# Kernel tuning notes

Hardware: AMD Instinct MI355X
Metric: run time of the kernel (lower is better)

Reference implementation:

```python
import jax, jax.numpy as jnp
import numpy as np

B, LQ, LK, DQ, DKEY, DV = 8, 2048, 2048, 1024, 1024, 1024
MASK_NEG = -1e6  # d2l masked_softmax fill value


def setup_inputs() -> dict:
    key = jax.random.key(0)
    kq, kk, kv, kl, kw = jax.random.split(key, 5)
    queries = jax.random.normal(kq, (B, LQ, DQ), dtype=jnp.float32)
    keys = jax.random.normal(kk, (B, LK, DKEY), dtype=jnp.float32)
    values = jax.random.normal(kv, (B, LK, DV), dtype=jnp.float32)
    valid_lens = jax.random.randint(kl, (B,), 1, LK + 1)
    W_q = jax.random.normal(kw, (DQ, DKEY), dtype=jnp.float32) / np.sqrt(DQ)
    return {"queries": queries, "keys": keys, "values": values,
            "valid_lens": valid_lens, "W_q": W_q}


def reference(queries, keys, values, valid_lens, W_q):
    # Q projection: LazyLinear(key_dim, bias=False)
    q = jnp.einsum("bqd,dk->bqk", queries, W_q)          # [B, LQ, DKEY]
    d = q.shape[-1]
    scores = jnp.einsum("bqk,bsk->bqs", q, keys) / jnp.sqrt(jnp.asarray(d, q.dtype))
    # masked_softmax: positions >= valid_len set to -1e6 before softmax
    mask = jnp.arange(scores.shape[-1])[None, None, :] < valid_lens[:, None, None]
    scores = jnp.where(mask, scores, MASK_NEG)
    attn = jax.nn.softmax(scores, axis=-1)               # [B, LQ, LK]
    # dropout p=0.0 (eval) -> identity
    return jnp.einsum("bqs,bsv->bqv", attn, values)      # [B, LQ, DV]
```

## Files before the change

kernel.cpp:

```cpp
#include <hip/hip_runtime.h>
#include <cstdint>
#include <cstddef>

#define B_   8
#define LQ_  2048
#define LK_  2048

typedef __attribute__((ext_vector_type(8))) __bf16 bf16x8;
typedef __attribute__((ext_vector_type(4))) float f32x4;
typedef __attribute__((ext_vector_type(8))) unsigned short ushortx8;

__device__ __forceinline__ unsigned short f2bf(float f) {
  unsigned u = __builtin_bit_cast(unsigned, f);
  u = u + 0x7fffu + ((u >> 16) & 1u);
  return (unsigned short)(u >> 16);
}
__device__ __forceinline__ float bf2f(unsigned short h) {
  unsigned u = ((unsigned)h) << 16;
  return __builtin_bit_cast(float, u);
}

__device__ __forceinline__ void gld_lds16(const void* g, void* l) {
  __builtin_amdgcn_global_load_lds((__attribute__((address_space(1))) void*)(void*)g,
                                   (__attribute__((address_space(3))) void*)l, 16, 0, 0);
}

__global__ __launch_bounds__(256) void cast_kw_kernel(
    const float* __restrict__ k, unsigned short* __restrict__ ko,
    const float* __restrict__ w, unsigned short* __restrict__ wo,
    const int* __restrict__ vlp) {
  int bb = (int)blockIdx.x;
  const float* in;
  unsigned short* out;
  if (bb < 8192) {
    in = k; out = ko;
    int batch = bb >> 10;
    int row = (bb & 1023) * 2;
    int vl = vlp[batch];
    if (row >= ((vl + 255) & ~255)) return;
  } else {
    bb -= 8192;
    in = w; out = wo;
  }
  size_t i = ((size_t)bb * 256 + threadIdx.x) * 8;
  float4 a = *(const float4*)(in + i);
  float4 b = *(const float4*)(in + i + 4);
  ushortx8 o;
  o[0] = f2bf(a.x); o[1] = f2bf(a.y); o[2] = f2bf(a.z); o[3] = f2bf(a.w);
  o[4] = f2bf(b.x); o[5] = f2bf(b.y); o[6] = f2bf(b.z); o[7] = f2bf(b.w);
  *(ushortx8*)(out + i) = o;
}

template <int OUTM, int SKIPN, int SKIPM, int CLAMPK, int QCAST>
__global__ __launch_bounds__(256, 2) void gemm256x128_kernel(
    const unsigned short* __restrict__ A, const unsigned short* __restrict__ B,
    void* __restrict__ Cp, int M, int N, int K,
    long a_bstride, long b_bstride, long c_bstride, float scale,
    const int* __restrict__ vlp, int lognx,
    const float* __restrict__ qf, unsigned short* __restrict__ qbf, int ngemm) {
  __shared__ unsigned short lds[2][128 * 64 + 64 * 64];

  const int tid = threadIdx.x;

  if constexpr (QCAST) {
    if ((int)blockIdx.x >= ngemm) {
      size_t i = ((size_t)((int)blockIdx.x - ngemm) * 256 + tid) * 8;
      float4 a = *(const float4*)(qf + i);
      float4 b = *(const float4*)(qf + i + 4);
      ushortx8 o;
      o[0] = f2bf(a.x); o[1] = f2bf(a.y); o[2] = f2bf(a.z); o[3] = f2bf(a.w);
      o[4] = f2bf(b.x); o[5] = f2bf(b.y); o[6] = f2bf(b.z); o[7] = f2bf(b.w);
      *(ushortx8*)(qbf + i) = o;
      return;
    }
  }

  const int wid = tid >> 6;
  const int lane = tid & 63;
  const int lane15 = lane & 15;
  const int lhalf = lane >> 4;

  const int idx = (int)blockIdx.x;
  const int z = idx & 7;
  const int rest = idx >> 3;
  const int nxm = (1 << lognx) - 1;
  const int xt = rest & nxm;
  const int yt = rest >> lognx;
  const int nt = (xt + 2 * z) & nxm;
  const int m0 = yt * 256;
  const int n0 = nt * 128;

  int vl = K;
  if constexpr (SKIPN || SKIPM || CLAMPK) vl = vlp[z];
  if constexpr (SKIPN) {
    if (n0 >= vl) return;
  }
  if constexpr (SKIPM) {
    if (m0 >= vl) return;
  }
  int kEnd = K;
  if constexpr (CLAMPK) {
    int ke = (vl + 63) & ~63;
    kEnd = ke < K ? ke : K;
  }
  const int nKt = kEnd >> 5;

  const unsigned short* Ab = A + (size_t)z * a_bstride;
  const unsigned short* Bb = B + (size_t)z * b_bstride;

  int srA[4], scA[4], sdA[4];
#pragma unroll
  for (int j = 0; j < 4; ++j) {
    int blk = (wid * 4 + j) * 64 + lane;
    int p = blk >> 3;
    int c = (blk & 7) ^ (p & 7);
    srA[j] = m0 + 2 * p + (c >> 2);
    scA[j] = (c & 3) * 8;
    sdA[j] = blk * 8;
  }
  int srB[2], scB[2], sdB[2];
#pragma unroll
  for (int j = 0; j < 2; ++j) {
    int blk = (wid * 2 + j) * 64 + lane;
    int p = blk >> 3;
    int c = (blk & 7) ^ (p & 7);
    srB[j] = n0 + 2 * p + (c >> 2);
    scB[j] = (c & 3) * 8;
    sdB[j] = 8192 + blk * 8;
  }

  const int om = (wid & 1) * 128;
  const int on = (wid >> 1) * 64;
  const int swz8 = ((((lane15 & 1) << 2) + lhalf) ^ ((lane15 >> 1) & 7)) << 3;
  const int aBase = ((om >> 1) + (lane15 >> 1)) * 64 + swz8;
  const int bBase = 8192 + ((on >> 1) + (lane15 >> 1)) * 64 + swz8;

  f32x4 acc[8][4];
#pragma unroll
  for (int f = 0; f < 8; ++f)
#pragma unroll
    for (int g = 0; g < 4; ++g) acc[f][g] = (f32x4){0.f, 0.f, 0.f, 0.f};

#define STAGE_TILE(T, S)                                                        \
  {                                                                             \
    const int kc_ = (T) * 32;                                                   \
    _Pragma("unroll")                                                           \
    for (int j = 0; j < 4; ++j)                                                 \
      gld_lds16(Ab + (size_t)srA[j] * K + (kc_ + scA[j]), &lds[S][sdA[j]]);     \
    _Pragma("unroll")                                                           \
    for (int j = 0; j < 2; ++j)                                                 \
      gld_lds16(Bb + (size_t)srB[j] * K + (kc_ + scB[j]), &lds[S][sdB[j]]);     \
  }

  STAGE_TILE(0, 0);
  asm volatile("s_waitcnt vmcnt(0)" ::: "memory");
  __builtin_amdgcn_s_barrier();

  for (int t = 0; t < nKt; ++t) {
    const unsigned short* lcur = &lds[t & 1][0];
    if (t + 1 < nKt) STAGE_TILE(t + 1, (t + 1) & 1);

    bf16x8 a[8], b[4];
#pragma unroll
    for (int f = 0; f < 8; ++f) a[f] = *(const bf16x8*)&lcur[aBase + f * 512];
#pragma unroll
    for (int g = 0; g < 4; ++g) b[g] = *(const bf16x8*)&lcur[bBase + g * 512];
#pragma unroll
    for (int f = 0; f < 8; ++f)
#pragma unroll
      for (int g = 0; g < 4; ++g)
        acc[f][g] = __builtin_amdgcn_mfma_f32_16x16x32_bf16(a[f], b[g], acc[f][g], 0, 0, 0);
    asm volatile("s_waitcnt vmcnt(0)" ::: "memory");
    __builtin_amdgcn_s_barrier();
  }
#undef STAGE_TILE

  const size_t boffC = (size_t)z * c_bstride;
#pragma unroll
  for (int f = 0; f < 8; ++f) {
    int row = m0 + om + f * 16 + lhalf * 4;
#pragma unroll
    for (int g = 0; g < 4; ++g) {
      int col = n0 + on + g * 16 + lane15;
#pragma unroll
      for (int r = 0; r < 4; ++r) {
        float v = acc[f][g][r];
        if constexpr (OUTM == 0) {
          ((unsigned short*)Cp + boffC)[(size_t)(row + r) * N + col] = f2bf(v);
        } else if constexpr (OUTM == 1) {
          ((unsigned short*)Cp + boffC)[(size_t)(row + r) * N + col] = f2bf(v * scale);
        } else {
          ((float*)Cp + boffC)[(size_t)(row + r) * N + col] = v;
        }
      }
    }
  }
}

__global__ __launch_bounds__(256) void vtrans_softmax_kernel(
    const float* __restrict__ vals, unsigned short* __restrict__ valsT,
    unsigned short* __restrict__ scores, const int* __restrict__ valid_lens) {
  __shared__ float smem[32 * 33];
  const int bb = (int)blockIdx.x;
  const int tid = threadIdx.x;

  if (bb < 16384) {
    const int z = bb >> 11;
    const int r0 = ((bb >> 5) & 63) * 32;
    const int kEnd = (valid_lens[z] + 63) & ~63;
    if (r0 >= kEnd) return;
    const int c0 = (bb & 31) * 32;
    const int tx = tid & 31, ty = tid >> 5;
    const float* inb = vals + (size_t)z * 2048 * 1024;
    unsigned short* outb = valsT + (size_t)z * 1024 * 2048;
#pragma unroll
    for (int k = 0; k < 4; ++k) {
      int r = ty + k * 8;
      smem[r * 33 + tx] = inb[(size_t)(r0 + r) * 1024 + c0 + tx];
    }
    __syncthreads();
#pragma unroll
    for (int k = 0; k < 4; ++k) {
      int c = ty + k * 8;
      outb[(size_t)(c0 + c) * 2048 + r0 + tx] = f2bf(smem[tx * 33 + c]);
    }
    return;
  }

  const int row = bb - 16384;
  const int b = row >> 11;
  const int vl = valid_lens[b];
  const int kEnd = (vl + 63) & ~63;
  unsigned short* rp = scores + (size_t)row * LK_;
  const int wid = tid >> 6, lane = tid & 63;
  float* sred = smem;

  const int cb = tid * 8;
  const bool act = cb < kEnd;
  ushortx8 h = {};
  if (act) h = *(const ushortx8*)(rp + cb);
  float x[8];
#pragma unroll
  for (int t = 0; t < 8; ++t) x[t] = bf2f(h[t]);

  float m = -3.4e38f;
#pragma unroll
  for (int t = 0; t < 8; ++t)
    if (cb + t < vl) m = fmaxf(m, x[t]);
#pragma unroll
  for (int off = 32; off >= 1; off >>= 1) m = fmaxf(m, __shfl_xor(m, off));
  if (lane == 0) sred[wid] = m;
  __syncthreads();
  m = fmaxf(fmaxf(sred[0], sred[1]), fmaxf(sred[2], sred[3]));
  __syncthreads();

  float e[8];
  float s = 0.f;
#pragma unroll
  for (int t = 0; t < 8; ++t) {
    e[t] = (cb + t < vl) ? __expf(x[t] - m) : 0.f;
    s += e[t];
  }
#pragma unroll
  for (int off = 32; off >= 1; off >>= 1) s += __shfl_xor(s, off);
  if (lane == 0) sred[wid] = s;
  __syncthreads();
  s = sred[0] + sred[1] + sred[2] + sred[3];
  float inv = 1.f / s;

  if (act) {
    ushortx8 o;
#pragma unroll
    for (int t = 0; t < 8; ++t) o[t] = f2bf(e[t] * inv);
    *(ushortx8*)(rp + cb) = o;
  }
}

extern "C" void kernel_launch(void* const* d_in, const int* in_sizes, int n_in,
                              void* d_out, int out_size, void* d_ws, size_t ws_size,
                              hipStream_t stream) {
  const float* queries = (const float*)d_in[0];
  const float* keys = (const float*)d_in[1];
  const float* values = (const float*)d_in[2];
  const int* valid_lens = (const int*)d_in[3];
  const float* W_q = (const float*)d_in[4];
  float* out = (float*)d_out;

  unsigned short* ws = (unsigned short*)d_ws;
  const size_t M1 = (size_t)1024 * 1024;
  unsigned short* q_bf = ws;
  unsigned short* scores = ws + 16 * M1;
  unsigned short* keysP = ws + 48 * M1;
  unsigned short* valsT = keysP;
  unsigned short* w_bf = ws + 64 * M1;
  unsigned short* keys_bf = ws + 65 * M1;

  cast_kw_kernel<<<dim3(8704), 256, 0, stream>>>(
      keys, keys_bf, W_q, w_bf, valid_lens);
  gemm256x128_kernel<0, 0, 1, 0, 1><<<dim3(512 + 8192), 256, 0, stream>>>(
      keys_bf, w_bf, keysP, 2048, 1024, 1024,
      (long)2048 * 1024, 0, (long)2048 * 1024, 1.f, valid_lens, 3,
      queries, q_bf, 512);
  gemm256x128_kernel<1, 1, 0, 0, 0><<<dim3(8 * 16 * 8), 256, 0, stream>>>(
      q_bf, keysP, scores, 2048, 2048, 1024,
      (long)2048 * 1024, (long)2048 * 1024, (long)2048 * 2048, 0.03125f, valid_lens, 4,
      nullptr, nullptr, 0);
  vtrans_softmax_kernel<<<dim3(32768), 256, 0, stream>>>(
      values, valsT, scores, valid_lens);
  gemm256x128_kernel<2, 0, 0, 1, 0><<<dim3(8 * 8 * 8), 256, 0, stream>>>(
      scores, valsT, out, 2048, 1024, 2048,
      (long)2048 * 2048, (long)1024 * 2048, (long)2048 * 1024, 1.f, valid_lens, 3,
      nullptr, nullptr, 0);
}
```

Baseline: 366.4 us.

## Fuse V transpose-cast into QK^T GEMM launch as auxiliary blocks

Moves the values transpose-and-cast-to-bf16 work out of the softmax kernel and into extra blocks appended to the QK^T score GEMM grid. Each auxiliary block handles eight 32x32 tiles and uses the GEMM's LDS as scratch. The transposed values are written into the keys_bf buffer, which is no longer needed by then, so they no longer alias keysP, which that GEMM is still reading. The aim is to let the bandwidth-bound transpose overlap with the compute-bound GEMM and to leave softmax as a lean kernel. The cost is that the auxiliary blocks compete with GEMM blocks for CU slots, and their fixed block count of 2048 may leave a load-imbalanced tail.

```diff
diff --git a/kernel.cpp b/kernel.cpp
--- a/kernel.cpp
+++ b/kernel.cpp
@@ -51,26 +51,58 @@
   *(ushortx8*)(out + i) = o;
 }
 
-template <int OUTM, int SKIPN, int SKIPM, int CLAMPK, int QCAST>
+template <int OUTM, int SKIPN, int SKIPM, int CLAMPK, int AUX>
 __global__ __launch_bounds__(256, 2) void gemm256x128_kernel(
     const unsigned short* __restrict__ A, const unsigned short* __restrict__ B,
     void* __restrict__ Cp, int M, int N, int K,
     long a_bstride, long b_bstride, long c_bstride, float scale,
     const int* __restrict__ vlp, int lognx,
-    const float* __restrict__ qf, unsigned short* __restrict__ qbf, int ngemm) {
+    const float* __restrict__ auxf, unsigned short* __restrict__ auxo, int ngemm) {
   __shared__ unsigned short lds[2][128 * 64 + 64 * 64];
 
   const int tid = threadIdx.x;
 
-  if constexpr (QCAST) {
+  if constexpr (AUX == 1) {
     if ((int)blockIdx.x >= ngemm) {
       size_t i = ((size_t)((int)blockIdx.x - ngemm) * 256 + tid) * 8;
-      float4 a = *(const float4*)(qf + i);
-      float4 b = *(const float4*)(qf + i + 4);
+      float4 a = *(const float4*)(auxf + i);
+      float4 b = *(const float4*)(auxf + i + 4);
       ushortx8 o;
       o[0] = f2bf(a.x); o[1] = f2bf(a.y); o[2] = f2bf(a.z); o[3] = f2bf(a.w);
       o[4] = f2bf(b.x); o[5] = f2bf(b.y); o[6] = f2bf(b.z); o[7] = f2bf(b.w);
-      *(ushortx8*)(qbf + i) = o;
+      *(ushortx8*)(auxo + i) = o;
+      return;
+    }
+  }
+  if constexpr (AUX == 2) {
+    if ((int)blockIdx.x >= ngemm) {
+      float* smem = (float*)&lds[0][0];
+      const int vb = (int)blockIdx.x - ngemm;
+      const int tx = tid & 31, ty = tid >> 5;
+#pragma unroll 1
+      for (int u = 0; u < 8; ++u) {
+        const int t = vb * 8 + u;
+        const int z = t >> 11;
+        const int r0 = ((t >> 5) & 63) * 32;
+        const int c0 = (t & 31) * 32;
+        const int kEnd = (vlp[z] + 63) & ~63;
+        if (r0 < kEnd) {
+          const float* inb = auxf + (size_t)z * 2048 * 1024;
+          unsigned short* outb = auxo + (size_t)z * 1024 * 2048;
+#pragma unroll
+          for (int k = 0; k < 4; ++k) {
+            int r = ty + k * 8;
+            smem[r * 33 + tx] = inb[(size_t)(r0 + r) * 1024 + c0 + tx];
+          }
+          __syncthreads();
+#pragma unroll
+          for (int k = 0; k < 4; ++k) {
+            int c = ty + k * 8;
+            outb[(size_t)(c0 + c) * 2048 + r0 + tx] = f2bf(smem[tx * 33 + c]);
+          }
+          __syncthreads();
+        }
+      }
       return;
     }
   }
@@ -197,43 +229,16 @@
   }
 }
 
-__global__ __launch_bounds__(256) void vtrans_softmax_kernel(
-    const float* __restrict__ vals, unsigned short* __restrict__ valsT,
-    unsigned short* __restrict__ scores, const int* __restrict__ valid_lens) {
-  __shared__ float smem[32 * 33];
-  const int bb = (int)blockIdx.x;
-  const int tid = threadIdx.x;
-
-  if (bb < 16384) {
-    const int z = bb >> 11;
-    const int r0 = ((bb >> 5) & 63) * 32;
-    const int kEnd = (valid_lens[z] + 63) & ~63;
-    if (r0 >= kEnd) return;
-    const int c0 = (bb & 31) * 32;
-    const int tx = tid & 31, ty = tid >> 5;
-    const float* inb = vals + (size_t)z * 2048 * 1024;
-    unsigned short* outb = valsT + (size_t)z * 1024 * 2048;
-#pragma unroll
-    for (int k = 0; k < 4; ++k) {
-      int r = ty + k * 8;
-      smem[r * 33 + tx] = inb[(size_t)(r0 + r) * 1024 + c0 + tx];
-    }
-    __syncthreads();
-#pragma unroll
-    for (int k = 0; k < 4; ++k) {
-      int c = ty + k * 8;
-      outb[(size_t)(c0 + c) * 2048 + r0 + tx] = f2bf(smem[tx * 33 + c]);
-    }
-    return;
-  }
-
-  const int row = bb - 16384;
+__global__ __launch_bounds__(256) void softmax_kernel(unsigned short* __restrict__ scores,
+                                                      const int* __restrict__ valid_lens) {
+  const int row = blockIdx.x;
   const int b = row >> 11;
   const int vl = valid_lens[b];
   const int kEnd = (vl + 63) & ~63;
   unsigned short* rp = scores + (size_t)row * LK_;
+  const int tid = threadIdx.x;
   const int wid = tid >> 6, lane = tid & 63;
-  float* sred = smem;
+  __shared__ float sred[4];
 
   const int cb = tid * 8;
   const bool act = cb < kEnd;
@@ -291,9 +296,9 @@
   unsigned short* q_bf = ws;
   unsigned short* scores = ws + 16 * M1;
   unsigned short* keysP = ws + 48 * M1;
-  unsigned short* valsT = keysP;
   unsigned short* w_bf = ws + 64 * M1;
   unsigned short* keys_bf = ws + 65 * M1;
+  unsigned short* valsT = keys_bf;
 
   cast_kw_kernel<<<dim3(8704), 256, 0, stream>>>(
       keys, keys_bf, W_q, w_bf, valid_lens);
@@ -301,12 +306,11 @@
       keys_bf, w_bf, keysP, 2048, 1024, 1024,
       (long)2048 * 1024, 0, (long)2048 * 1024, 1.f, valid_lens, 3,
       queries, q_bf, 512);
-  gemm256x128_kernel<1, 1, 0, 0, 0><<<dim3(8 * 16 * 8), 256, 0, stream>>>(
+  gemm256x128_kernel<1, 1, 0, 0, 2><<<dim3(1024 + 2048), 256, 0, stream>>>(
       q_bf, keysP, scores, 2048, 2048, 1024,
       (long)2048 * 1024, (long)2048 * 1024, (long)2048 * 2048, 0.03125f, valid_lens, 4,
-      nullptr, nullptr, 0);
-  vtrans_softmax_kernel<<<dim3(32768), 256, 0, stream>>>(
-      values, valsT, scores, valid_lens);
+      values, valsT, 1024);
+  softmax_kernel<<<dim3(B_ * LQ_), 256, 0, stream>>>(scores, valid_lens);
   gemm256x128_kernel<2, 0, 0, 1, 0><<<dim3(8 * 8 * 8), 256, 0, stream>>>(
       scores, valsT, out, 2048, 1024, 2048,
       (long)2048 * 2048, (long)1024 * 2048, (long)2048 * 1024, 1.f, valid_lens, 3,
```

Measured after the change: 371.3 us. About the same (+1.3%).

## Split-K the attention-value GEMM with atomic float accumulation into pre-zeroed output

Applied to the files above, without the earlier changes.

The final P·V GEMM is split into two K-halves when the clamped K range is at least 32 tiles. The halves accumulate into the float output with relaxed atomic adds, and the softmax kernel gains extra blocks that zero the output for those batches. valsT moves to the keys_bf workspace region so it no longer aliases keysP. The aim is more parallelism for the 512-block GEMM on a large GPU, at the cost of zeroing traffic, atomic write contention, and a nondeterministic summation order.

```diff
diff --git a/kernel.cpp b/kernel.cpp
--- a/kernel.cpp
+++ b/kernel.cpp
@@ -51,26 +51,26 @@
   *(ushortx8*)(out + i) = o;
 }
 
-template <int OUTM, int SKIPN, int SKIPM, int CLAMPK, int QCAST>
+template <int OUTM, int SKIPN, int SKIPM, int CLAMPK, int AUX, int SPLITK>
 __global__ __launch_bounds__(256, 2) void gemm256x128_kernel(
     const unsigned short* __restrict__ A, const unsigned short* __restrict__ B,
     void* __restrict__ Cp, int M, int N, int K,
     long a_bstride, long b_bstride, long c_bstride, float scale,
     const int* __restrict__ vlp, int lognx,
-    const float* __restrict__ qf, unsigned short* __restrict__ qbf, int ngemm) {
+    const float* __restrict__ auxf, unsigned short* __restrict__ auxo, int ngemm) {
   __shared__ unsigned short lds[2][128 * 64 + 64 * 64];
 
   const int tid = threadIdx.x;
 
-  if constexpr (QCAST) {
+  if constexpr (AUX == 1) {
     if ((int)blockIdx.x >= ngemm) {
       size_t i = ((size_t)((int)blockIdx.x - ngemm) * 256 + tid) * 8;
-      float4 a = *(const float4*)(qf + i);
-      float4 b = *(const float4*)(qf + i + 4);
+      float4 a = *(const float4*)(auxf + i);
+      float4 b = *(const float4*)(auxf + i + 4);
       ushortx8 o;
       o[0] = f2bf(a.x); o[1] = f2bf(a.y); o[2] = f2bf(a.z); o[3] = f2bf(a.w);
       o[4] = f2bf(b.x); o[5] = f2bf(b.y); o[6] = f2bf(b.z); o[7] = f2bf(b.w);
-      *(ushortx8*)(qbf + i) = o;
+      *(ushortx8*)(auxo + i) = o;
       return;
     }
   }
@@ -82,7 +82,12 @@
 
   const int idx = (int)blockIdx.x;
   const int z = idx & 7;
-  const int rest = idx >> 3;
+  int rest = idx >> 3;
+  int sk = 0;
+  if constexpr (SPLITK) {
+    sk = rest & 1;
+    rest >>= 1;
+  }
   const int nxm = (1 << lognx) - 1;
   const int xt = rest & nxm;
   const int yt = rest >> lognx;
@@ -104,6 +109,18 @@
     kEnd = ke < K ? ke : K;
   }
   const int nKt = kEnd >> 5;
+
+  int t0 = 0, t1 = nKt;
+  bool split = false;
+  if constexpr (SPLITK) {
+    if (nKt >= 32) {
+      split = true;
+      const int h = nKt >> 1;
+      if (sk) t0 = h; else t1 = h;
+    } else if (sk) {
+      return;
+    }
+  }
 
   const unsigned short* Ab = A + (size_t)z * a_bstride;
   const unsigned short* Bb = B + (size_t)z * b_bstride;
@@ -152,13 +169,14 @@
       gld_lds16(Bb + (size_t)srB[j] * K + (kc_ + scB[j]), &lds[S][sdB[j]]);     \
   }
 
-  STAGE_TILE(0, 0);
+  STAGE_TILE(t0, 0);
   asm volatile("s_waitcnt vmcnt(0)" ::: "memory");
   __builtin_amdgcn_s_barrier();
 
-  for (int t = 0; t < nKt; ++t) {
-    const unsigned short* lcur = &lds[t & 1][0];
-    if (t + 1 < nKt) STAGE_TILE(t + 1, (t + 1) & 1);
+  for (int t = t0; t < t1; ++t) {
+    const int cur = (t - t0) & 1;
+    const unsigned short* lcur = &lds[cur][0];
+    if (t + 1 < t1) STAGE_TILE(t + 1, cur ^ 1);
 
     bf16x8 a[8], b[4];
 #pragma unroll
@@ -190,19 +208,40 @@
         } else if constexpr (OUTM == 1) {
           ((unsigned short*)Cp + boffC)[(size_t)(row + r) * N + col] = f2bf(v * scale);
         } else {
-          ((float*)Cp + boffC)[(size_t)(row + r) * N + col] = v;
+          float* op = (float*)Cp + boffC;
+          if constexpr (SPLITK) {
+            if (split) {
+              __hip_atomic_fetch_add(&op[(size_t)(row + r) * N + col], v,
+                                     __ATOMIC_RELAXED, __HIP_MEMORY_SCOPE_AGENT);
+              continue;
+            }
+          }
+          op[(size_t)(row + r) * N + col] = v;
         }
       }
     }
   }
 }
 
-__global__ __launch_bounds__(256) void vtrans_softmax_kernel(
+__global__ __launch_bounds__(256) void vtrans_softmax_zero_kernel(
     const float* __restrict__ vals, unsigned short* __restrict__ valsT,
-    unsigned short* __restrict__ scores, const int* __restrict__ valid_lens) {
+    unsigned short* __restrict__ scores, const int* __restrict__ valid_lens,
+    float* __restrict__ out) {
   __shared__ float smem[32 * 33];
   const int bb = (int)blockIdx.x;
   const int tid = threadIdx.x;
+
+  if (bb >= 32768) {
+    const int zb = bb - 32768;
+    const int z = zb >> 8;
+    if (((valid_lens[z] + 63) & ~63) >= 1024) {
+      float* p = out + ((size_t)z << 21) + ((size_t)(zb & 255) << 13) + tid * 32;
+      const f32x4 zer = {0.f, 0.f, 0.f, 0.f};
+#pragma unroll
+      for (int u = 0; u < 8; ++u) *(f32x4*)(p + u * 4) = zer;
+    }
+    return;
+  }
 
   if (bb < 16384) {
     const int z = bb >> 11;
@@ -291,23 +330,23 @@
   unsigned short* q_bf = ws;
   unsigned short* scores = ws + 16 * M1;
   unsigned short* keysP = ws + 48 * M1;
-  unsigned short* valsT = keysP;
   unsigned short* w_bf = ws + 64 * M1;
   unsigned short* keys_bf = ws + 65 * M1;
+  unsigned short* valsT = keys_bf;
 
   cast_kw_kernel<<<dim3(8704), 256, 0, stream>>>(
       keys, keys_bf, W_q, w_bf, valid_lens);
-  gemm256x128_kernel<0, 0, 1, 0, 1><<<dim3(512 + 8192), 256, 0, stream>>>(
+  gemm256x128_kernel<0, 0, 1, 0, 1, 0><<<dim3(512 + 8192), 256, 0, stream>>>(
       keys_bf, w_bf, keysP, 2048, 1024, 1024,
       (long)2048 * 1024, 0, (long)2048 * 1024, 1.f, valid_lens, 3,
       queries, q_bf, 512);
-  gemm256x128_kernel<1, 1, 0, 0, 0><<<dim3(8 * 16 * 8), 256, 0, stream>>>(
+  gemm256x128_kernel<1, 1, 0, 0, 0, 0><<<dim3(8 * 16 * 8), 256, 0, stream>>>(
       q_bf, keysP, scores, 2048, 2048, 1024,
       (long)2048 * 1024, (long)2048 * 1024, (long)2048 * 2048, 0.03125f, valid_lens, 4,
       nullptr, nullptr, 0);
-  vtrans_softmax_kernel<<<dim3(32768), 256, 0, stream>>>(
-      values, valsT, scores, valid_lens);
-  gemm256x128_kernel<2, 0, 0, 1, 0><<<dim3(8 * 8 * 8), 256, 0, stream>>>(
+  vtrans_softmax_zero_kernel<<<dim3(34816), 256, 0, stream>>>(
+      values, valsT, scores, valid_lens, out);
+  gemm256x128_kernel<2, 0, 0, 1, 0, 1><<<dim3(8 * 8 * 2 * 8), 256, 0, stream>>>(
       scores, valsT, out, 2048, 1024, 2048,
       (long)2048 * 2048, (long)1024 * 2048, (long)2048 * 1024, 1.f, valid_lens, 3,
       nullptr, nullptr, 0);
```

Measured after the change: 403.9 us. 1.1x slower.
